# Kernel optimization log

Measured on AMD Instinct MI355X. Metric: run time of the kernel, lower is better.

Reference implementation:

```python
import jax, jax.numpy as jnp
import numpy as np

N_NODES = 20000
N_EDGES = 320000
IN_F = 256
HID = 64
OUT_F = 64
EDGE_F = 16
HEADS = 4
NUM_CLASSES = 10
NUM_GRAPHS = 40
ALPHA = 0.2  # LeakyReLU negative slope


def _xavier(key, shape):
    fan_in, fan_out = shape[0], shape[-1]
    std = 1.414 * np.sqrt(2.0 / (fan_in + fan_out))
    return jax.random.normal(key, shape, dtype=jnp.float32) * std


def setup_inputs() -> dict:
    key = jax.random.key(0)
    ks = jax.random.split(key, 12)
    x = jax.random.normal(ks[0], (N_NODES, IN_F), dtype=jnp.float32)
    edge_index = jax.random.randint(ks[1], (2, N_EDGES), 0, N_NODES, dtype=jnp.int32)
    edge_attr = jax.random.uniform(ks[2], (N_EDGES, EDGE_F), dtype=jnp.float32)
    batch = jnp.sort(jax.random.randint(ks[3], (N_NODES,), 0, NUM_GRAPHS, dtype=jnp.int32))
    # layer 0: in=IN_F, heads=HEADS, out=HID, concat
    W0 = _xavier(ks[4], (IN_F, HEADS * HID))
    a0 = _xavier(ks[5], (HEADS, 2 * HID + EDGE_F))
    # layer 1: in=HID*HEADS, heads=HEADS, out=HID, concat
    W1 = _xavier(ks[6], (HID * HEADS, HEADS * HID))
    a1 = _xavier(ks[7], (HEADS, 2 * HID + EDGE_F))
    # layer 2: in=HID*HEADS, heads=1, out=OUT_F, mean over heads
    W2 = _xavier(ks[8], (HID * HEADS, 1 * OUT_F))
    a2 = _xavier(ks[9], (1, 2 * OUT_F + EDGE_F))
    cls_w = _xavier(ks[10], (OUT_F, NUM_CLASSES))
    cls_b = jnp.zeros((NUM_CLASSES,), dtype=jnp.float32)
    return {"x": x, "edge_index": edge_index, "edge_attr": edge_attr, "batch": batch,
            "W0": W0, "a0": a0, "W1": W1, "a1": a1, "W2": W2, "a2": a2,
            "cls_w": cls_w, "cls_b": cls_b}


def gat_layer(h, W, a, edge_index, edge_attr, heads, out_f, concat):
    n = h.shape[0]
    Wh = (h @ W).reshape(n, heads, out_f)              # [N,H,D]
    src, dst = edge_index[0], edge_index[1]
    a_i, a_j, a_e = a[:, :out_f], a[:, out_f:2 * out_f], a[:, 2 * out_f:]
    # per-node head scores, gathered per edge (equivalent to concat + dot with a)
    s_i = jnp.einsum('nhd,hd->nh', Wh, a_i)            # [N,H]
    s_j = jnp.einsum('nhd,hd->nh', Wh, a_j)            # [N,H]
    s_e = edge_attr @ a_e.T                            # [E,H]
    e = s_i[src] + s_j[dst] + s_e                      # [E,H]
    e = jnp.where(e > 0, e, ALPHA * e)                 # LeakyReLU
    # NB: faithful to source — softmax over the HEADS dim (dim=1), not per-node
    att = jax.nn.softmax(e, axis=1)                    # [E,H]
    msg = att[:, :, None] * Wh[dst]                    # [E,H,D]
    h_prime = jax.ops.segment_sum(msg, src, num_segments=n)  # scatter-add to src
    if concat:
        return jax.nn.elu(h_prime.reshape(n, heads * out_f))
    return h_prime.mean(axis=1)


def reference(x, edge_index, edge_attr, batch, W0, a0, W1, a1, W2, a2, cls_w, cls_b):
    h = gat_layer(x, W0, a0, edge_index, edge_attr, HEADS, HID, True)
    h = gat_layer(h, W1, a1, edge_index, edge_attr, HEADS, HID, True)
    h = gat_layer(h, W2, a2, edge_index, edge_attr, 1, OUT_F, False)
    # global mean pool over graphs
    sums = jax.ops.segment_sum(h, batch, num_segments=NUM_GRAPHS)
    cnts = jax.ops.segment_sum(jnp.ones((h.shape[0],), h.dtype), batch, num_segments=NUM_GRAPHS)
    pooled = sums / jnp.maximum(cnts, 1.0)[:, None]
    logits = pooled @ cls_w + cls_b
    return jax.nn.log_softmax(logits, axis=1)
```

## Files before the change

kernel.cpp:

```cpp
#include <hip/hip_runtime.h>
#include <hip/hip_bf16.h>
#include <math.h>

#define N_NODES 20000
#define N_EDGES 320000
#define IN_F 256
#define HID 64
#define HEADS 4
#define OUT_F 64
#define EDGE_F 16
#define NUM_CLASSES 10
#define NUM_GRAPHS 40
#define LRELU_ALPHA 0.2f

typedef short bf16x8 __attribute__((ext_vector_type(8)));
typedef unsigned short u16x8 __attribute__((ext_vector_type(8)));
typedef float f32x4 __attribute__((ext_vector_type(4)));

static __device__ __forceinline__ float bf2f(unsigned short u) {
    union { unsigned int i; float f; } v; v.i = ((unsigned int)u) << 16; return v.f;
}
static __device__ __forceinline__ unsigned short f2bf(float f) {
    union { float f; unsigned int i; } v; v.f = f;
    unsigned int r = v.i + 0x7FFF + ((v.i >> 16) & 1);
    return (unsigned short)(r >> 16);
}
static __device__ __forceinline__ float eluf(float a) {
    return a > 0.f ? a : __expf(a) - 1.0f;
}

__global__ void prep_kernel(const float* __restrict__ W0, const float* __restrict__ W1,
                            const float* __restrict__ W2, unsigned short* __restrict__ W0b,
                            unsigned short* __restrict__ W1b, unsigned short* __restrict__ W2b,
                            int* __restrict__ cnt) {
    int b = blockIdx.x;
    if (b < 144) {
        int i = b * 256 + threadIdx.x;
        const float* src; unsigned short* dst; int off;
        if (i < 16384)      { src = W0; dst = W0b; off = i; }
        else if (i < 32768) { src = W1; dst = W1b; off = i - 16384; }
        else                { src = W2; dst = W2b; off = i - 32768; }
        float4 v = ((const float4*)src)[off];
        ushort4 o;
        o.x = f2bf(v.x); o.y = f2bf(v.y); o.z = f2bf(v.z); o.w = f2bf(v.w);
        ((ushort4*)dst)[off] = o;
    } else {
        int j = (b - 144) * 256 + threadIdx.x;
        if (j < N_NODES / 4) ((int4*)cnt)[j] = make_int4(0, 0, 0, 0);
    }
}

__global__ void count_kernel(const int* __restrict__ src, int* __restrict__ cnt) {
    int e = blockIdx.x * blockDim.x + threadIdx.x;
    if (e < N_EDGES) atomicAdd(&cnt[src[e]], 1);
}

__global__ __launch_bounds__(1024) void scan_kernel(const int* __restrict__ cnt,
                                                    int* __restrict__ row_ptr,
                                                    int* __restrict__ cursor) {
    __shared__ int wsum[16];
    __shared__ int carry_s;
    int t = threadIdx.x;
    int lane = t & 63, wave = t >> 6;
    if (t == 0) { carry_s = 0; row_ptr[0] = 0; }
    __syncthreads();
    for (int base = 0; base < N_NODES; base += 1024) {
        int idx = base + t;
        int x0 = (idx < N_NODES) ? cnt[idx] : 0;
        int x = x0;
#pragma unroll
        for (int off = 1; off < 64; off <<= 1) {
            int y = __shfl_up(x, off, 64);
            if (lane >= off) x += y;
        }
        if (lane == 63) wsum[wave] = x;
        __syncthreads();
        if (wave == 0 && lane < 16) {
            int s = wsum[lane];
#pragma unroll
            for (int off = 1; off < 16; off <<= 1) {
                int y = __shfl_up(s, off, 64);
                if (lane >= off) s += y;
            }
            wsum[lane] = s;
        }
        __syncthreads();
        int waveoff = (wave > 0) ? wsum[wave - 1] : 0;
        int carry = carry_s;
        if (idx < N_NODES) {
            int incl = x + waveoff + carry;
            row_ptr[idx + 1] = incl;
            cursor[idx] = incl - x0;
        }
        __syncthreads();
        if (t == 0) carry_s = carry + wsum[15];
        __syncthreads();
    }
}

__global__ void scatter_kernel(const int* __restrict__ src, const int* __restrict__ dst,
                               const float* __restrict__ ea, const float* __restrict__ a0,
                               const float* __restrict__ a1, int* __restrict__ cursor,
                               int* __restrict__ dstp, float* __restrict__ se0,
                               float* __restrict__ se1) {
    __shared__ float ae[2][4][16];
    int tid = threadIdx.x;
    if (tid < 64) ae[0][tid >> 4][tid & 15] = a0[(tid >> 4) * 144 + 128 + (tid & 15)];
    else if (tid < 128) { int t = tid - 64; ae[1][t >> 4][t & 15] = a1[(t >> 4) * 144 + 128 + (t & 15)]; }
    __syncthreads();
    int e = blockIdx.x * blockDim.x + tid;
    if (e >= N_EDGES) return;
    int s = src[e];
    int pos = atomicAdd(&cursor[s], 1);
    dstp[pos] = dst[e];
    float x[16];
#pragma unroll
    for (int k = 0; k < 16; k += 4) {
        float4 v = *(const float4*)(ea + (size_t)e * 16 + k);
        x[k] = v.x; x[k + 1] = v.y; x[k + 2] = v.z; x[k + 3] = v.w;
    }
    float4 o0 = make_float4(0.f, 0.f, 0.f, 0.f), o1 = o0;
#pragma unroll
    for (int k = 0; k < 16; ++k) {
        o0.x += x[k] * ae[0][0][k]; o0.y += x[k] * ae[0][1][k];
        o0.z += x[k] * ae[0][2][k]; o0.w += x[k] * ae[0][3][k];
        o1.x += x[k] * ae[1][0][k]; o1.y += x[k] * ae[1][1][k];
        o1.z += x[k] * ae[1][2][k]; o1.w += x[k] * ae[1][3][k];
    }
    ((float4*)se0)[pos] = o0;
    ((float4*)se1)[pos] = o1;
}

template <bool AF32, bool SCORES>
__global__ __launch_bounds__(256) void gemm_bf16(const void* __restrict__ Aptr,
                                                 const unsigned short* __restrict__ B,
                                                 unsigned short* __restrict__ C,
                                                 const float* __restrict__ avec,
                                                 float* __restrict__ si, float* __restrict__ sj,
                                                 int M, int N, int K) {
    __shared__ unsigned short As[128][40];
    __shared__ unsigned short Bs[64][40];
    __shared__ unsigned short Cs[128][72];
    __shared__ float sa[128];
    int tid = threadIdx.x;
    if (SCORES && tid < 128) sa[tid] = avec[blockIdx.y * 144 + tid];
    int bm = blockIdx.x * 128, bn = blockIdx.y * 64;
    int w = tid >> 6, l = tid & 63;
    int wr = w * 32;
    int lr = l & 15, lk = (l >> 4) * 8;
    f32x4 acc[2][4] = {};
    int ar = tid >> 1, akc = (tid & 1) * 16;
    int bk = tid >> 3, bn8 = tid & 7, bnc = bn8 * 8;

    for (int k0 = 0; k0 < K; k0 += 32) {
        bf16x8 av0 = {}, av1 = {};
        if (bm + ar < M) {
            if constexpr (AF32) {
                const float* Af = (const float*)Aptr + (size_t)(bm + ar) * K + k0 + akc;
                float4 f0 = ((const float4*)Af)[0];
                float4 f1 = ((const float4*)Af)[1];
                float4 f2 = ((const float4*)Af)[2];
                float4 f3 = ((const float4*)Af)[3];
                av0[0] = (short)f2bf(f0.x); av0[1] = (short)f2bf(f0.y);
                av0[2] = (short)f2bf(f0.z); av0[3] = (short)f2bf(f0.w);
                av0[4] = (short)f2bf(f1.x); av0[5] = (short)f2bf(f1.y);
                av0[6] = (short)f2bf(f1.z); av0[7] = (short)f2bf(f1.w);
                av1[0] = (short)f2bf(f2.x); av1[1] = (short)f2bf(f2.y);
                av1[2] = (short)f2bf(f2.z); av1[3] = (short)f2bf(f2.w);
                av1[4] = (short)f2bf(f3.x); av1[5] = (short)f2bf(f3.y);
                av1[6] = (short)f2bf(f3.z); av1[7] = (short)f2bf(f3.w);
            } else {
                const unsigned short* Ab = (const unsigned short*)Aptr + (size_t)(bm + ar) * K + k0 + akc;
                av0 = *(const bf16x8*)Ab;
                av1 = *(const bf16x8*)(Ab + 8);
            }
        }
        *(bf16x8*)&As[ar][akc] = av0;
        *(bf16x8*)&As[ar][akc + 8] = av1;
        bf16x8 bv = *(const bf16x8*)(B + (size_t)(k0 + bk) * N + bn + bnc);
#pragma unroll
        for (int j = 0; j < 8; ++j) {
            int jj = (j + bn8) & 7;
            Bs[bnc + jj][bk] = (unsigned short)bv[jj];
        }
        __syncthreads();
        bf16x8 a0 = *(const bf16x8*)&As[wr + lr][lk];
        bf16x8 a1 = *(const bf16x8*)&As[wr + 16 + lr][lk];
        bf16x8 b0 = *(const bf16x8*)&Bs[lr][lk];
        bf16x8 b1 = *(const bf16x8*)&Bs[16 + lr][lk];
        bf16x8 b2 = *(const bf16x8*)&Bs[32 + lr][lk];
        bf16x8 b3 = *(const bf16x8*)&Bs[48 + lr][lk];
        acc[0][0] = __builtin_amdgcn_mfma_f32_16x16x32_bf16(a0, b0, acc[0][0], 0, 0, 0);
        acc[0][1] = __builtin_amdgcn_mfma_f32_16x16x32_bf16(a0, b1, acc[0][1], 0, 0, 0);
        acc[0][2] = __builtin_amdgcn_mfma_f32_16x16x32_bf16(a0, b2, acc[0][2], 0, 0, 0);
        acc[0][3] = __builtin_amdgcn_mfma_f32_16x16x32_bf16(a0, b3, acc[0][3], 0, 0, 0);
        acc[1][0] = __builtin_amdgcn_mfma_f32_16x16x32_bf16(a1, b0, acc[1][0], 0, 0, 0);
        acc[1][1] = __builtin_amdgcn_mfma_f32_16x16x32_bf16(a1, b1, acc[1][1], 0, 0, 0);
        acc[1][2] = __builtin_amdgcn_mfma_f32_16x16x32_bf16(a1, b2, acc[1][2], 0, 0, 0);
        acc[1][3] = __builtin_amdgcn_mfma_f32_16x16x32_bf16(a1, b3, acc[1][3], 0, 0, 0);
        __syncthreads();
    }
#pragma unroll
    for (int i = 0; i < 2; ++i)
#pragma unroll
        for (int j = 0; j < 4; ++j)
#pragma unroll
            for (int r = 0; r < 4; ++r)
                Cs[wr + i * 16 + (l >> 4) * 4 + r][j * 16 + (l & 15)] = f2bf(acc[i][j][r]);
    __syncthreads();
    {
        int row = tid >> 3, cc = (tid & 7) * 8;
#pragma unroll
        for (int p = 0; p < 4; ++p, row += 32) {
            if (bm + row < M) {
                bf16x8 o = *(const bf16x8*)&Cs[row][cc];
                *(bf16x8*)(C + (size_t)(bm + row) * N + bn + cc) = o;
            }
        }
    }
    if (SCORES) {
        int r = tid >> 1, half = tid & 1;
        float s0 = 0.f, s1 = 0.f;
#pragma unroll
        for (int k = 0; k < 32; ++k) {
            float f = bf2f(Cs[r][half * 32 + k]);
            s0 += f * sa[half * 32 + k];
            s1 += f * sa[64 + half * 32 + k];
        }
        s0 += __shfl_xor(s0, 1, 64);
        s1 += __shfl_xor(s1, 1, 64);
        if (half == 0 && bm + r < M) {
            si[(size_t)(bm + r) * 4 + blockIdx.y] = s0;
            sj[(size_t)(bm + r) * 4 + blockIdx.y] = s1;
        }
    }
}

__global__ __launch_bounds__(256) void edge_agg_concat(
    const unsigned short* __restrict__ Whb, const float* __restrict__ sev,
    const float* __restrict__ si, const float* __restrict__ sj,
    const int* __restrict__ row_ptr, const int* __restrict__ dstp,
    unsigned short* __restrict__ out) {
    int v = blockIdx.x * 4 + (threadIdx.x >> 6);
    if (v >= N_NODES) return;
    int l = threadIdx.x & 63;
    int slot = l >> 4, p = l & 15;
    int beg = row_ptr[v], end = row_ptr[v + 1];
    float4 si4 = ((const float4*)si)[v];
    float acc0[8] = {}, acc1[8] = {};
    int i = beg + slot;
    int u_n = 0;
    float4 se_n = make_float4(0.f, 0.f, 0.f, 0.f), sj_n = se_n;
    if (i < end) {
        u_n = dstp[i];
        se_n = ((const float4*)sev)[i];
        sj_n = ((const float4*)sj)[u_n];
    }
    for (; i < end; i += 4) {
        int u = u_n;
        float4 se4 = se_n, sj4 = sj_n;
        if (i + 4 < end) {
            u_n = dstp[i + 4];
            se_n = ((const float4*)sev)[i + 4];
            sj_n = ((const float4*)sj)[u_n];
        }
        float t0 = si4.x + sj4.x + se4.x;
        float t1 = si4.y + sj4.y + se4.y;
        float t2 = si4.z + sj4.z + se4.z;
        float t3 = si4.w + sj4.w + se4.w;
        t0 = t0 > 0.f ? t0 : LRELU_ALPHA * t0;
        t1 = t1 > 0.f ? t1 : LRELU_ALPHA * t1;
        t2 = t2 > 0.f ? t2 : LRELU_ALPHA * t2;
        t3 = t3 > 0.f ? t3 : LRELU_ALPHA * t3;
        float m = fmaxf(fmaxf(t0, t1), fmaxf(t2, t3));
        float p0 = __expf(t0 - m), p1 = __expf(t1 - m), p2 = __expf(t2 - m), p3 = __expf(t3 - m);
        float inv = 1.0f / (p0 + p1 + p2 + p3);
        const unsigned short* row = Whb + (size_t)u * 256;
        u16x8 w0 = *(const u16x8*)(row + p * 8);
        u16x8 w1 = *(const u16x8*)(row + 128 + p * 8);
        float atA = ((p & 8) ? p1 : p0) * inv;
        float atB = ((p & 8) ? p3 : p2) * inv;
#pragma unroll
        for (int j = 0; j < 8; ++j) acc0[j] += atA * bf2f(w0[j]);
#pragma unroll
        for (int j = 0; j < 8; ++j) acc1[j] += atB * bf2f(w1[j]);
    }
#pragma unroll
    for (int j = 0; j < 8; ++j) {
        acc0[j] += __shfl_xor(acc0[j], 16, 64);
        acc0[j] += __shfl_xor(acc0[j], 32, 64);
        acc1[j] += __shfl_xor(acc1[j], 16, 64);
        acc1[j] += __shfl_xor(acc1[j], 32, 64);
    }
    if (slot == 0) {
        u16x8 o0, o1;
#pragma unroll
        for (int j = 0; j < 8; ++j) {
            o0[j] = f2bf(eluf(acc0[j]));
            o1[j] = f2bf(eluf(acc1[j]));
        }
        *(u16x8*)(out + (size_t)v * 256 + p * 8) = o0;
        *(u16x8*)(out + (size_t)v * 256 + 128 + p * 8) = o1;
    }
}

__global__ __launch_bounds__(256) void edge_agg_single(
    const unsigned short* __restrict__ Whb, const int* __restrict__ row_ptr,
    const int* __restrict__ dstp, float* __restrict__ out) {
    int v = blockIdx.x * 4 + (threadIdx.x >> 6);
    if (v >= N_NODES) return;
    int l = threadIdx.x & 63;
    int slot = l >> 3, p = l & 7;
    int beg = row_ptr[v], end = row_ptr[v + 1];
    float acc[8] = {};
    int i = beg + slot;
    int u_n = 0;
    if (i < end) u_n = dstp[i];
    for (; i < end; i += 8) {
        int u = u_n;
        if (i + 8 < end) u_n = dstp[i + 8];
        u16x8 w = *(const u16x8*)(Whb + (size_t)u * 64 + p * 8);
#pragma unroll
        for (int j = 0; j < 8; ++j) acc[j] += bf2f(w[j]);
    }
#pragma unroll
    for (int j = 0; j < 8; ++j) {
        acc[j] += __shfl_xor(acc[j], 8, 64);
        acc[j] += __shfl_xor(acc[j], 16, 64);
        acc[j] += __shfl_xor(acc[j], 32, 64);
    }
    if (l < 8) {
        float4 o0 = make_float4(acc[0], acc[1], acc[2], acc[3]);
        float4 o1 = make_float4(acc[4], acc[5], acc[6], acc[7]);
        *(float4*)(out + (size_t)v * 64 + p * 8) = o0;
        *(float4*)(out + (size_t)v * 64 + p * 8 + 4) = o1;
    }
}

__global__ __launch_bounds__(1024) void pool_kernel(const float* __restrict__ h3,
                                                    const int* __restrict__ batch,
                                                    float* __restrict__ pooled) {
    int g = blockIdx.x;
    int lane = threadIdx.x & 63;
    int wave = threadIdx.x >> 6;
    int lo = 0, hi = N_NODES;
    while (lo < hi) { int mid = (lo + hi) >> 1; if (batch[mid] < g) lo = mid + 1; else hi = mid; }
    int start = lo;
    lo = start; hi = N_NODES;
    while (lo < hi) { int mid = (lo + hi) >> 1; if (batch[mid] < g + 1) lo = mid + 1; else hi = mid; }
    int endi = lo;
    float s = 0.f;
    for (int v = start + wave; v < endi; v += 16) s += h3[(size_t)v * 64 + lane];
    __shared__ float red[16][64];
    red[wave][lane] = s;
    __syncthreads();
    if (wave == 0) {
        float t = red[0][lane];
#pragma unroll
        for (int w = 1; w < 16; ++w) t += red[w][lane];
        float c = (float)((endi - start) > 1 ? (endi - start) : 1);
        pooled[g * 64 + lane] = t / c;
    }
}

__global__ void classify_kernel(const float* __restrict__ pooled, const float* __restrict__ cw,
                                const float* __restrict__ cb, float* __restrict__ out) {
    int g = threadIdx.x;
    if (g >= NUM_GRAPHS) return;
    float lg[NUM_CLASSES];
#pragma unroll
    for (int c = 0; c < NUM_CLASSES; ++c) lg[c] = cb[c];
    for (int d = 0; d < OUT_F; ++d) {
        float p = pooled[g * 64 + d];
#pragma unroll
        for (int c = 0; c < NUM_CLASSES; ++c) lg[c] += p * cw[d * NUM_CLASSES + c];
    }
    float m = lg[0];
#pragma unroll
    for (int c = 1; c < NUM_CLASSES; ++c) m = fmaxf(m, lg[c]);
    float s = 0.f;
#pragma unroll
    for (int c = 0; c < NUM_CLASSES; ++c) s += expf(lg[c] - m);
    float lse = m + logf(s);
#pragma unroll
    for (int c = 0; c < NUM_CLASSES; ++c) out[g * NUM_CLASSES + c] = lg[c] - lse;
}

extern "C" void kernel_launch(void* const* d_in, const int* in_sizes, int n_in,
                              void* d_out, int out_size, void* d_ws, size_t ws_size,
                              hipStream_t stream) {
    const float* x   = (const float*)d_in[0];
    const int*   ei  = (const int*)d_in[1];
    const float* ea  = (const float*)d_in[2];
    const int* batch = (const int*)d_in[3];
    const float* W0  = (const float*)d_in[4];
    const float* a0  = (const float*)d_in[5];
    const float* W1  = (const float*)d_in[6];
    const float* a1  = (const float*)d_in[7];
    const float* W2  = (const float*)d_in[8];
    const float* cw  = (const float*)d_in[10];
    const float* cb  = (const float*)d_in[11];
    float* out = (float*)d_out;

    const int* srcg = ei;
    const int* dstg = ei + N_EDGES;

    char* ws = (char*)d_ws;
    size_t off = 0;
    auto alloc = [&](size_t bytes) -> char* {
        char* p = ws + off;
        off += (bytes + 255) & ~(size_t)255;
        return p;
    };
    unsigned short* W0b  = (unsigned short*)alloc(256 * 256 * 2);
    unsigned short* W1b  = (unsigned short*)alloc(256 * 256 * 2);
    unsigned short* W2b  = (unsigned short*)alloc(256 * 64 * 2);
    unsigned short* Whb  = (unsigned short*)alloc((size_t)N_NODES * 256 * 2);
    unsigned short* hAb  = (unsigned short*)alloc((size_t)N_NODES * 256 * 2);
    unsigned short* hBb  = (unsigned short*)alloc((size_t)N_NODES * 256 * 2);
    unsigned short* Wh2b = (unsigned short*)alloc((size_t)N_NODES * 64 * 2);
    float* si   = (float*)alloc((size_t)N_NODES * HEADS * 4);
    float* sj   = (float*)alloc((size_t)N_NODES * HEADS * 4);
    float* se0  = (float*)alloc((size_t)N_EDGES * HEADS * 4);
    float* se1  = (float*)alloc((size_t)N_EDGES * HEADS * 4);
    int* row_ptr = (int*)alloc((N_NODES + 1) * 4);
    int* cursor  = (int*)alloc(N_NODES * 4);
    int* cnt  = (int*)alloc(N_NODES * 4);
    int* dstp = (int*)alloc(N_EDGES * 4);
    float* h3 = (float*)alloc((size_t)N_NODES * 64 * 4);
    float* pooled = (float*)alloc(NUM_GRAPHS * 64 * 4);

    prep_kernel<<<144 + (N_NODES / 4 + 255) / 256, 256, 0, stream>>>(W0, W1, W2, W0b, W1b, W2b, cnt);

    count_kernel<<<(N_EDGES + 255) / 256, 256, 0, stream>>>(srcg, cnt);
    scan_kernel<<<1, 1024, 0, stream>>>(cnt, row_ptr, cursor);
    scatter_kernel<<<(N_EDGES + 255) / 256, 256, 0, stream>>>(srcg, dstg, ea, a0, a1, cursor,
                                                              dstp, se0, se1);

    dim3 ggrid((N_NODES + 127) / 128, 4);
    dim3 ggrid2((N_NODES + 127) / 128, 1);
    int agb = (N_NODES + 3) / 4;

    gemm_bf16<true, true><<<ggrid, 256, 0, stream>>>(x, W0b, Whb, a0, si, sj, N_NODES, 256, 256);
    edge_agg_concat<<<agb, 256, 0, stream>>>(Whb, se0, si, sj, row_ptr, dstp, hAb);

    gemm_bf16<false, true><<<ggrid, 256, 0, stream>>>(hAb, W1b, Whb, a1, si, sj, N_NODES, 256, 256);
    edge_agg_concat<<<agb, 256, 0, stream>>>(Whb, se1, si, sj, row_ptr, dstp, hBb);

    gemm_bf16<false, false><<<ggrid2, 256, 0, stream>>>(hBb, W2b, Wh2b, nullptr, nullptr, nullptr,
                                                        N_NODES, 64, 256);
    edge_agg_single<<<agb, 256, 0, stream>>>(Wh2b, row_ptr, dstp, h3);

    pool_kernel<<<NUM_GRAPHS, 1024, 0, stream>>>(h3, batch, pooled);
    classify_kernel<<<1, 64, 0, stream>>>(pooled, cw, cb, out);
}
```

Measured before the change: 207.8 us.

## Preload full B tile in GEMM, widen edge aggregation, interleave edge scores

```diff
diff --git a/kernel.cpp b/kernel.cpp
--- a/kernel.cpp
+++ b/kernel.cpp
@@ -50,9 +50,15 @@
     }
 }
 
-__global__ void count_kernel(const int* __restrict__ src, int* __restrict__ cnt) {
-    int e = blockIdx.x * blockDim.x + threadIdx.x;
-    if (e < N_EDGES) atomicAdd(&cnt[src[e]], 1);
+__global__ void count_kernel(const int4* __restrict__ src4, int* __restrict__ cnt) {
+    int i = blockIdx.x * blockDim.x + threadIdx.x;
+    if (i < N_EDGES / 4) {
+        int4 s = src4[i];
+        atomicAdd(&cnt[s.x], 1);
+        atomicAdd(&cnt[s.y], 1);
+        atomicAdd(&cnt[s.z], 1);
+        atomicAdd(&cnt[s.w], 1);
+    }
 }
 
 __global__ __launch_bounds__(1024) void scan_kernel(const int* __restrict__ cnt,
@@ -101,8 +107,7 @@
 __global__ void scatter_kernel(const int* __restrict__ src, const int* __restrict__ dst,
                                const float* __restrict__ ea, const float* __restrict__ a0,
                                const float* __restrict__ a1, int* __restrict__ cursor,
-                               int* __restrict__ dstp, float* __restrict__ se0,
-                               float* __restrict__ se1) {
+                               int* __restrict__ dstp, float* __restrict__ se01) {
     __shared__ float ae[2][4][16];
     int tid = threadIdx.x;
     if (tid < 64) ae[0][tid >> 4][tid & 15] = a0[(tid >> 4) * 144 + 128 + (tid & 15)];
@@ -127,8 +132,8 @@
         o1.x += x[k] * ae[1][0][k]; o1.y += x[k] * ae[1][1][k];
         o1.z += x[k] * ae[1][2][k]; o1.w += x[k] * ae[1][3][k];
     }
-    ((float4*)se0)[pos] = o0;
-    ((float4*)se1)[pos] = o1;
+    ((float4*)se01)[(size_t)pos * 2]     = o0;
+    ((float4*)se01)[(size_t)pos * 2 + 1] = o1;
 }
 
 template <bool AF32, bool SCORES>
@@ -138,9 +143,8 @@
                                                  const float* __restrict__ avec,
                                                  float* __restrict__ si, float* __restrict__ sj,
                                                  int M, int N, int K) {
+    __shared__ unsigned short Bs[64][264];
     __shared__ unsigned short As[128][40];
-    __shared__ unsigned short Bs[64][40];
-    __shared__ unsigned short Cs[128][72];
     __shared__ float sa[128];
     int tid = threadIdx.x;
     if (SCORES && tid < 128) sa[tid] = avec[blockIdx.y * 144 + tid];
@@ -150,7 +154,16 @@
     int lr = l & 15, lk = (l >> 4) * 8;
     f32x4 acc[2][4] = {};
     int ar = tid >> 1, akc = (tid & 1) * 16;
-    int bk = tid >> 3, bn8 = tid & 7, bnc = bn8 * 8;
+    int bn8 = tid & 7, bnc = bn8 * 8;
+
+    for (int kk = tid >> 3; kk < K; kk += 32) {
+        bf16x8 bv = *(const bf16x8*)(B + (size_t)kk * N + bn + bnc);
+#pragma unroll
+        for (int j = 0; j < 8; ++j) {
+            int jj = (j + bn8) & 7;
+            Bs[bnc + jj][kk] = (unsigned short)bv[jj];
+        }
+    }
 
     for (int k0 = 0; k0 < K; k0 += 32) {
         bf16x8 av0 = {}, av1 = {};
@@ -177,19 +190,13 @@
         }
         *(bf16x8*)&As[ar][akc] = av0;
         *(bf16x8*)&As[ar][akc + 8] = av1;
-        bf16x8 bv = *(const bf16x8*)(B + (size_t)(k0 + bk) * N + bn + bnc);
-#pragma unroll
-        for (int j = 0; j < 8; ++j) {
-            int jj = (j + bn8) & 7;
-            Bs[bnc + jj][bk] = (unsigned short)bv[jj];
-        }
         __syncthreads();
         bf16x8 a0 = *(const bf16x8*)&As[wr + lr][lk];
         bf16x8 a1 = *(const bf16x8*)&As[wr + 16 + lr][lk];
-        bf16x8 b0 = *(const bf16x8*)&Bs[lr][lk];
-        bf16x8 b1 = *(const bf16x8*)&Bs[16 + lr][lk];
-        bf16x8 b2 = *(const bf16x8*)&Bs[32 + lr][lk];
-        bf16x8 b3 = *(const bf16x8*)&Bs[48 + lr][lk];
+        bf16x8 b0 = *(const bf16x8*)&Bs[lr][k0 + lk];
+        bf16x8 b1 = *(const bf16x8*)&Bs[16 + lr][k0 + lk];
+        bf16x8 b2 = *(const bf16x8*)&Bs[32 + lr][k0 + lk];
+        bf16x8 b3 = *(const bf16x8*)&Bs[48 + lr][k0 + lk];
         acc[0][0] = __builtin_amdgcn_mfma_f32_16x16x32_bf16(a0, b0, acc[0][0], 0, 0, 0);
         acc[0][1] = __builtin_amdgcn_mfma_f32_16x16x32_bf16(a0, b1, acc[0][1], 0, 0, 0);
         acc[0][2] = __builtin_amdgcn_mfma_f32_16x16x32_bf16(a0, b2, acc[0][2], 0, 0, 0);
@@ -200,68 +207,70 @@
         acc[1][3] = __builtin_amdgcn_mfma_f32_16x16x32_bf16(a1, b3, acc[1][3], 0, 0, 0);
         __syncthreads();
     }
+
 #pragma unroll
     for (int i = 0; i < 2; ++i)
 #pragma unroll
-        for (int j = 0; j < 4; ++j)
-#pragma unroll
-            for (int r = 0; r < 4; ++r)
-                Cs[wr + i * 16 + (l >> 4) * 4 + r][j * 16 + (l & 15)] = f2bf(acc[i][j][r]);
-    __syncthreads();
-    {
-        int row = tid >> 3, cc = (tid & 7) * 8;
-#pragma unroll
-        for (int p = 0; p < 4; ++p, row += 32) {
-            if (bm + row < M) {
-                bf16x8 o = *(const bf16x8*)&Cs[row][cc];
-                *(bf16x8*)(C + (size_t)(bm + row) * N + bn + cc) = o;
+        for (int r = 0; r < 4; ++r) {
+            int row = bm + wr + i * 16 + (l >> 4) * 4 + r;
+            if (row < M) {
+#pragma unroll
+                for (int j = 0; j < 4; ++j)
+                    C[(size_t)row * N + bn + j * 16 + lr] = f2bf(acc[i][j][r]);
             }
         }
-    }
+
     if (SCORES) {
-        int r = tid >> 1, half = tid & 1;
-        float s0 = 0.f, s1 = 0.f;
-#pragma unroll
-        for (int k = 0; k < 32; ++k) {
-            float f = bf2f(Cs[r][half * 32 + k]);
-            s0 += f * sa[half * 32 + k];
-            s1 += f * sa[64 + half * 32 + k];
-        }
-        s0 += __shfl_xor(s0, 1, 64);
-        s1 += __shfl_xor(s1, 1, 64);
-        if (half == 0 && bm + r < M) {
-            si[(size_t)(bm + r) * 4 + blockIdx.y] = s0;
-            sj[(size_t)(bm + r) * 4 + blockIdx.y] = s1;
-        }
+#pragma unroll
+        for (int i = 0; i < 2; ++i)
+#pragma unroll
+            for (int r = 0; r < 4; ++r) {
+                float s0 = 0.f, s1 = 0.f;
+#pragma unroll
+                for (int j = 0; j < 4; ++j) {
+                    float f = acc[i][j][r];
+                    s0 += f * sa[j * 16 + lr];
+                    s1 += f * sa[64 + j * 16 + lr];
+                }
+                s0 += __shfl_xor(s0, 1, 64); s0 += __shfl_xor(s0, 2, 64);
+                s0 += __shfl_xor(s0, 4, 64); s0 += __shfl_xor(s0, 8, 64);
+                s1 += __shfl_xor(s1, 1, 64); s1 += __shfl_xor(s1, 2, 64);
+                s1 += __shfl_xor(s1, 4, 64); s1 += __shfl_xor(s1, 8, 64);
+                int row = bm + wr + i * 16 + (l >> 4) * 4 + r;
+                if (lr == 0 && row < M) {
+                    si[(size_t)row * 4 + blockIdx.y] = s0;
+                    sj[(size_t)row * 4 + blockIdx.y] = s1;
+                }
+            }
     }
 }
 
 __global__ __launch_bounds__(256) void edge_agg_concat(
-    const unsigned short* __restrict__ Whb, const float* __restrict__ sev,
+    const unsigned short* __restrict__ Whb, const float4* __restrict__ sev,
     const float* __restrict__ si, const float* __restrict__ sj,
     const int* __restrict__ row_ptr, const int* __restrict__ dstp,
     unsigned short* __restrict__ out) {
     int v = blockIdx.x * 4 + (threadIdx.x >> 6);
     if (v >= N_NODES) return;
     int l = threadIdx.x & 63;
-    int slot = l >> 4, p = l & 15;
+    int slot = l >> 3, p = l & 7;
     int beg = row_ptr[v], end = row_ptr[v + 1];
     float4 si4 = ((const float4*)si)[v];
-    float acc0[8] = {}, acc1[8] = {};
+    float acc0[8] = {}, acc1[8] = {}, acc2[8] = {}, acc3[8] = {};
     int i = beg + slot;
     int u_n = 0;
     float4 se_n = make_float4(0.f, 0.f, 0.f, 0.f), sj_n = se_n;
     if (i < end) {
         u_n = dstp[i];
-        se_n = ((const float4*)sev)[i];
+        se_n = sev[(size_t)i * 2];
         sj_n = ((const float4*)sj)[u_n];
     }
-    for (; i < end; i += 4) {
+    for (; i < end; i += 8) {
         int u = u_n;
         float4 se4 = se_n, sj4 = sj_n;
-        if (i + 4 < end) {
-            u_n = dstp[i + 4];
-            se_n = ((const float4*)sev)[i + 4];
+        if (i + 8 < end) {
+            u_n = dstp[i + 8];
+            se_n = sev[(size_t)(i + 8) * 2];
             sj_n = ((const float4*)sj)[u_n];
         }
         float t0 = si4.x + sj4.x + se4.x;
@@ -275,32 +284,49 @@
         float m = fmaxf(fmaxf(t0, t1), fmaxf(t2, t3));
         float p0 = __expf(t0 - m), p1 = __expf(t1 - m), p2 = __expf(t2 - m), p3 = __expf(t3 - m);
         float inv = 1.0f / (p0 + p1 + p2 + p3);
-        const unsigned short* row = Whb + (size_t)u * 256;
-        u16x8 w0 = *(const u16x8*)(row + p * 8);
-        u16x8 w1 = *(const u16x8*)(row + 128 + p * 8);
-        float atA = ((p & 8) ? p1 : p0) * inv;
-        float atB = ((p & 8) ? p3 : p2) * inv;
-#pragma unroll
-        for (int j = 0; j < 8; ++j) acc0[j] += atA * bf2f(w0[j]);
-#pragma unroll
-        for (int j = 0; j < 8; ++j) acc1[j] += atB * bf2f(w1[j]);
+        float at0 = p0 * inv, at1 = p1 * inv, at2 = p2 * inv, at3 = p3 * inv;
+        const unsigned short* row = Whb + (size_t)u * 256 + p * 8;
+        u16x8 w0 = *(const u16x8*)(row);
+        u16x8 w1 = *(const u16x8*)(row + 64);
+        u16x8 w2 = *(const u16x8*)(row + 128);
+        u16x8 w3 = *(const u16x8*)(row + 192);
+#pragma unroll
+        for (int j = 0; j < 8; ++j) {
+            acc0[j] += at0 * bf2f(w0[j]);
+            acc1[j] += at1 * bf2f(w1[j]);
+            acc2[j] += at2 * bf2f(w2[j]);
+            acc3[j] += at3 * bf2f(w3[j]);
+        }
     }
 #pragma unroll
     for (int j = 0; j < 8; ++j) {
+        acc0[j] += __shfl_xor(acc0[j], 8, 64);
         acc0[j] += __shfl_xor(acc0[j], 16, 64);
         acc0[j] += __shfl_xor(acc0[j], 32, 64);
+        acc1[j] += __shfl_xor(acc1[j], 8, 64);
         acc1[j] += __shfl_xor(acc1[j], 16, 64);
         acc1[j] += __shfl_xor(acc1[j], 32, 64);
-    }
-    if (slot == 0) {
-        u16x8 o0, o1;
+        acc2[j] += __shfl_xor(acc2[j], 8, 64);
+        acc2[j] += __shfl_xor(acc2[j], 16, 64);
+        acc2[j] += __shfl_xor(acc2[j], 32, 64);
+        acc3[j] += __shfl_xor(acc3[j], 8, 64);
+        acc3[j] += __shfl_xor(acc3[j], 16, 64);
+        acc3[j] += __shfl_xor(acc3[j], 32, 64);
+    }
+    if (l < 8) {
+        u16x8 o0, o1, o2, o3;
 #pragma unroll
         for (int j = 0; j < 8; ++j) {
             o0[j] = f2bf(eluf(acc0[j]));
             o1[j] = f2bf(eluf(acc1[j]));
-        }
-        *(u16x8*)(out + (size_t)v * 256 + p * 8) = o0;
-        *(u16x8*)(out + (size_t)v * 256 + 128 + p * 8) = o1;
+            o2[j] = f2bf(eluf(acc2[j]));
+            o3[j] = f2bf(eluf(acc3[j]));
+        }
+        unsigned short* ob = out + (size_t)v * 256 + p * 8;
+        *(u16x8*)(ob)       = o0;
+        *(u16x8*)(ob + 64)  = o1;
+        *(u16x8*)(ob + 128) = o2;
+        *(u16x8*)(ob + 192) = o3;
     }
 }
 
@@ -421,8 +447,7 @@
     unsigned short* Wh2b = (unsigned short*)alloc((size_t)N_NODES * 64 * 2);
     float* si   = (float*)alloc((size_t)N_NODES * HEADS * 4);
     float* sj   = (float*)alloc((size_t)N_NODES * HEADS * 4);
-    float* se0  = (float*)alloc((size_t)N_EDGES * HEADS * 4);
-    float* se1  = (float*)alloc((size_t)N_EDGES * HEADS * 4);
+    float* se01 = (float*)alloc((size_t)N_EDGES * 8 * 4);
     int* row_ptr = (int*)alloc((N_NODES + 1) * 4);
     int* cursor  = (int*)alloc(N_NODES * 4);
     int* cnt  = (int*)alloc(N_NODES * 4);
@@ -432,20 +457,20 @@
 
     prep_kernel<<<144 + (N_NODES / 4 + 255) / 256, 256, 0, stream>>>(W0, W1, W2, W0b, W1b, W2b, cnt);
 
-    count_kernel<<<(N_EDGES + 255) / 256, 256, 0, stream>>>(srcg, cnt);
+    count_kernel<<<(N_EDGES / 4 + 255) / 256, 256, 0, stream>>>((const int4*)srcg, cnt);
     scan_kernel<<<1, 1024, 0, stream>>>(cnt, row_ptr, cursor);
     scatter_kernel<<<(N_EDGES + 255) / 256, 256, 0, stream>>>(srcg, dstg, ea, a0, a1, cursor,
-                                                              dstp, se0, se1);
+                                                              dstp, se01);
 
     dim3 ggrid((N_NODES + 127) / 128, 4);
     dim3 ggrid2((N_NODES + 127) / 128, 1);
     int agb = (N_NODES + 3) / 4;
 
     gemm_bf16<true, true><<<ggrid, 256, 0, stream>>>(x, W0b, Whb, a0, si, sj, N_NODES, 256, 256);
-    edge_agg_concat<<<agb, 256, 0, stream>>>(Whb, se0, si, sj, row_ptr, dstp, hAb);
+    edge_agg_concat<<<agb, 256, 0, stream>>>(Whb, (const float4*)se01, si, sj, row_ptr, dstp, hAb);
 
     gemm_bf16<false, true><<<ggrid, 256, 0, stream>>>(hAb, W1b, Whb, a1, si, sj, N_NODES, 256, 256);
-    edge_agg_concat<<<agb, 256, 0, stream>>>(Whb, se1, si, sj, row_ptr, dstp, hBb);
+    edge_agg_concat<<<agb, 256, 0, stream>>>(Whb, (const float4*)se01 + 1, si, sj, row_ptr, dstp, hBb);
 
     gemm_bf16<false, false><<<ggrid2, 256, 0, stream>>>(hBb, W2b, Wh2b, nullptr, nullptr, nullptr,
                                                         N_NODES, 64, 256);
```

New measurement: 218.9 us. +5.4%, slower.
